# Performance work log

Measured on AMD Instinct MI355X. Metric: run time of the kernel, lower is better.

## Reference

```python
import jax, jax.numpy as jnp
import numpy as np

B, S, H, D = 2, 2048, 32, 128
DM = H * D  # 4096
SCALE = D ** -0.5


def setup_inputs() -> dict:
    key = jax.random.key(0)
    ks = jax.random.split(key, 7)
    std = DM ** -0.5
    return {
        "q": jax.random.normal(ks[0], (B, S, DM), dtype=jnp.float32),
        "k": jax.random.normal(ks[1], (B, S, DM), dtype=jnp.float32),
        "v": jax.random.normal(ks[2], (B, S, DM), dtype=jnp.float32),
        # torch nn.Linear weights are [out_features, in_features]
        "Wq": jax.random.normal(ks[3], (DM, DM), dtype=jnp.float32) * std,
        "Wk": jax.random.normal(ks[4], (DM, DM), dtype=jnp.float32) * std,
        "Wv": jax.random.normal(ks[5], (DM, DM), dtype=jnp.float32) * std,
        "Wo": jax.random.normal(ks[6], (DM, DM), dtype=jnp.float32) * std,
    }


def reference(q, k, v, Wq, Wk, Wv, Wo):
    # Linear: y = x @ W^T (no bias, qkv_bias=False)
    qp = q @ Wq.T  # [B,S,DM]
    kp = k @ Wk.T
    vp = v @ Wv.T
    # [B,S,DM] -> [B,H,S,D]
    qh = qp.reshape(B, S, H, D).transpose(0, 2, 1, 3)
    kh = kp.reshape(B, S, H, D).transpose(0, 2, 1, 3)
    vh = vp.reshape(B, S, H, D).transpose(0, 2, 1, 3)
    # scaled dot-product attention (no mask; attn_mask default None)
    scores = jnp.einsum("bhqd,bhkd->bhqk", qh, kh) * SCALE  # [B,H,S,S]
    probs = jax.nn.softmax(scores, axis=-1)
    ctx = jnp.einsum("bhqk,bhkd->bhqd", probs, vh)  # [B,H,S,D]
    ctx = ctx.transpose(0, 2, 1, 3).reshape(B, S, DM)
    return ctx @ Wo.T  # [B,S,DM]
```

## Files before the change

### kernel.cpp

```cpp
#include <hip/hip_runtime.h>
#include <hip/hip_bf16.h>
#include <stdint.h>


using u16 = unsigned short;
using u32 = unsigned int;

typedef __attribute__((ext_vector_type(8))) short bf16x8;
typedef __attribute__((ext_vector_type(8))) u16 u16x8;
typedef __attribute__((ext_vector_type(4))) float f32x4;

#define MFMA_BF16(A, B, C) __builtin_amdgcn_mfma_f32_16x16x32_bf16((A), (B), (C), 0, 0, 0)

static constexpr int kS = 2048, kDM = 4096, kD = 128;
static constexpr size_t kMat = (size_t)4096 * 4096;
static constexpr float kScaleLog2e = 0.08838834764831845f * 1.44269504088896340736f;

static __device__ __forceinline__ void gload_lds16(const u16* g, u16* l) {
  __builtin_amdgcn_global_load_lds((const __attribute__((address_space(1))) void*)g,
                                   (__attribute__((address_space(3))) void*)l, 16, 0, 0);
}

static __device__ __forceinline__ u16 f2bf(float f) {
  u32 u = __float_as_uint(f);
  u32 r = u + 0x7FFFu + ((u >> 16) & 1u);
  return (u16)(r >> 16);
}

static __device__ __forceinline__ float bf2f(u16 x) {
  return __uint_as_float((u32)x << 16);
}

static __device__ __forceinline__ u16 nbf(float f) {
  union { __hip_bfloat16 h; u16 u; } cv;
  cv.h = __float2bfloat16(f);
  return cv.u;
}

static __device__ __forceinline__ u16x8 cvt8(float4 a, float4 b) {
  u16x8 r;
  r[0] = f2bf(a.x); r[1] = f2bf(a.y); r[2] = f2bf(a.z); r[3] = f2bf(a.w);
  r[4] = f2bf(b.x); r[5] = f2bf(b.y); r[6] = f2bf(b.z); r[7] = f2bf(b.w);
  return r;
}

__global__ __launch_bounds__(256) void cvt_kernel(
    const float* __restrict__ s0, const float* __restrict__ s1,
    const float* __restrict__ s2, const float* __restrict__ s3,
    const float* __restrict__ s4, const float* __restrict__ s5,
    const float* __restrict__ s6, u16* __restrict__ dst) {
  const int y = blockIdx.y;
  const float* s = (y == 0) ? s0 : (y == 1) ? s1 : (y == 2) ? s2 : (y == 3) ? s3
                  : (y == 4) ? s4 : (y == 5) ? s5 : s6;
  u16* d = dst + (size_t)y * kMat;
  const size_t nchunk = kMat / 8;
  const size_t step = (size_t)gridDim.x * 256;
  for (size_t c = (size_t)blockIdx.x * 256 + threadIdx.x; c < nchunk; c += step) {
    const float* p = s + c * 8;
    float4 a = *(const float4*)p;
    float4 b = *(const float4*)(p + 4);
    *(u16x8*)(d + c * 8) = cvt8(a, b);
  }
}

template <bool TRANS, bool OUT_F32>
static __device__ __forceinline__ void gemm256(const u16* __restrict__ X,
                                               const u16* __restrict__ W,
                                               void* __restrict__ Yv,
                                               u16* __restrict__ lds) {
  constexpr int NT = kDM / 64;
  const int tid = threadIdx.x;
  const int lane = tid & 63;
  const int w = tid >> 6;
  const int fr = lane & 15;
  const int fq = lane >> 4;
  const int wr = w >> 2;
  const int wc = w & 3;
  const int m0 = blockIdx.y * 256;
  const int n0 = blockIdx.x * 256;

  const int srow = tid >> 3;
  const int scol = ((tid & 7) ^ (srow & 7)) * 8;
  const u16* Xrow = X + (size_t)(m0 + srow) * kDM + scol;
  const u16* Wrow = W + (size_t)(n0 + srow) * kDM + scol;
  const int w512 = w * 512;

  const int rBb = wc * 64 + fr;
  const int rAb = wr * 128 + fr;
  const int swz = fr & 7;

  f32x4 acc[8][4] = {};

#define STAGE2(ROWP, qrow, k0, ldq)                                       \
  do {                                                                    \
    gload_lds16((ROWP) + (size_t)(qrow) * kDM + (k0), &lds[(ldq) + w512]); \
    gload_lds16((ROWP) + (size_t)((qrow) + 64) * kDM + (k0),              \
                &lds[(ldq) + 4096 + w512]);                               \
  } while (0)

  STAGE2(Wrow, 0, 0, 0);
  STAGE2(Wrow, 128, 0, 8192);
  STAGE2(Xrow, 0, 0, 16384);
  STAGE2(Xrow, 128, 0, 24576);
  STAGE2(Wrow, 0, 64, 32768);
  STAGE2(Wrow, 128, 64, 32768 + 8192);
  STAGE2(Xrow, 0, 64, 32768 + 16384);
  asm volatile("s_waitcnt vmcnt(6)" ::: "memory");
  __builtin_amdgcn_s_barrier();

  for (int t = 0; t < NT; ++t) {
    const int d = t & 1;
    const int Boff = d * 32768;
    const int Aoff = Boff + 16384;
    bf16x8 bfr[4][2], af[8][2];

#pragma unroll
    for (int nf = 0; nf < 4; ++nf)
#pragma unroll
      for (int ks = 0; ks < 2; ++ks)
        bfr[nf][ks] = *(const bf16x8*)&lds[Boff + (rBb + nf * 16) * 64 +
                                           (((ks * 4 + fq) ^ swz) * 8)];
#pragma unroll
    for (int mi = 0; mi < 4; ++mi)
#pragma unroll
      for (int ks = 0; ks < 2; ++ks)
        af[mi][ks] = *(const bf16x8*)&lds[Aoff + (rAb + mi * 16) * 64 +
                                          (((ks * 4 + fq) ^ swz) * 8)];
    if (t + 1 < NT) STAGE2(Xrow, 128, (t + 1) * 64, ((t + 1) & 1) * 32768 + 24576);
    __builtin_amdgcn_s_barrier();
    __builtin_amdgcn_s_setprio(1);
#pragma unroll
    for (int mi = 0; mi < 2; ++mi)
#pragma unroll
      for (int nf = 0; nf < 4; ++nf)
#pragma unroll
        for (int ks = 0; ks < 2; ++ks)
          acc[mi][nf] = TRANS ? MFMA_BF16(bfr[nf][ks], af[mi][ks], acc[mi][nf])
                              : MFMA_BF16(af[mi][ks], bfr[nf][ks], acc[mi][nf]);
    __builtin_amdgcn_s_setprio(0);
    __builtin_amdgcn_s_barrier();

#pragma unroll
    for (int mi = 4; mi < 6; ++mi)
#pragma unroll
      for (int ks = 0; ks < 2; ++ks)
        af[mi][ks] = *(const bf16x8*)&lds[Aoff + (rAb + mi * 16) * 64 +
                                          (((ks * 4 + fq) ^ swz) * 8)];
    if (t + 2 < NT) STAGE2(Wrow, 0, (t + 2) * 64, d * 32768 + 0);
    __builtin_amdgcn_s_barrier();
    __builtin_amdgcn_s_setprio(1);
#pragma unroll
    for (int mi = 2; mi < 4; ++mi)
#pragma unroll
      for (int nf = 0; nf < 4; ++nf)
#pragma unroll
        for (int ks = 0; ks < 2; ++ks)
          acc[mi][nf] = TRANS ? MFMA_BF16(bfr[nf][ks], af[mi][ks], acc[mi][nf])
                              : MFMA_BF16(af[mi][ks], bfr[nf][ks], acc[mi][nf]);
    __builtin_amdgcn_s_setprio(0);
    __builtin_amdgcn_s_barrier();

#pragma unroll
    for (int mi = 6; mi < 8; ++mi)
#pragma unroll
      for (int ks = 0; ks < 2; ++ks)
        af[mi][ks] = *(const bf16x8*)&lds[Aoff + (rAb + mi * 16) * 64 +
                                          (((ks * 4 + fq) ^ swz) * 8)];
    if (t + 2 < NT) STAGE2(Wrow, 128, (t + 2) * 64, d * 32768 + 8192);
    __builtin_amdgcn_s_barrier();
    __builtin_amdgcn_s_setprio(1);
#pragma unroll
    for (int mi = 4; mi < 6; ++mi)
#pragma unroll
      for (int nf = 0; nf < 4; ++nf)
#pragma unroll
        for (int ks = 0; ks < 2; ++ks)
          acc[mi][nf] = TRANS ? MFMA_BF16(bfr[nf][ks], af[mi][ks], acc[mi][nf])
                              : MFMA_BF16(af[mi][ks], bfr[nf][ks], acc[mi][nf]);
    __builtin_amdgcn_s_setprio(0);
    asm volatile("s_waitcnt lgkmcnt(0)" ::: "memory");
    __builtin_amdgcn_s_barrier();

    if (t + 2 < NT) STAGE2(Xrow, 0, (t + 2) * 64, d * 32768 + 16384);
    __builtin_amdgcn_s_barrier();
    __builtin_amdgcn_s_setprio(1);
#pragma unroll
    for (int mi = 6; mi < 8; ++mi)
#pragma unroll
      for (int nf = 0; nf < 4; ++nf)
#pragma unroll
        for (int ks = 0; ks < 2; ++ks)
          acc[mi][nf] = TRANS ? MFMA_BF16(bfr[nf][ks], af[mi][ks], acc[mi][nf])
                              : MFMA_BF16(af[mi][ks], bfr[nf][ks], acc[mi][nf]);
    __builtin_amdgcn_s_setprio(0);
    if (t + 2 < NT)
      asm volatile("s_waitcnt vmcnt(6)" ::: "memory");
    else
      asm volatile("s_waitcnt vmcnt(0)" ::: "memory");
    __builtin_amdgcn_s_barrier();
  }
#undef STAGE2

#pragma unroll
  for (int mi = 0; mi < 8; ++mi)
#pragma unroll
    for (int nf = 0; nf < 4; ++nf) {
      int row, col;
      if constexpr (TRANS) {
        row = n0 + wc * 64 + nf * 16 + fq * 4;
        col = m0 + wr * 128 + mi * 16 + fr;
      } else {
        row = m0 + wr * 128 + mi * 16 + fq * 4;
        col = n0 + wc * 64 + nf * 16 + fr;
      }
      if constexpr (OUT_F32) {
        float* yp = (float*)Yv + (size_t)row * kDM + col;
#pragma unroll
        for (int i = 0; i < 4; ++i) yp[(size_t)i * kDM] = acc[mi][nf][i];
      } else {
        u16* yp = (u16*)Yv + (size_t)row * kDM + col;
#pragma unroll
        for (int i = 0; i < 4; ++i) yp[(size_t)i * kDM] = f2bf(acc[mi][nf][i]);
      }
    }
}

__global__ __launch_bounds__(512, 2) void proj_qk256_kernel(const u16* __restrict__ wsb,
                                                            u16* __restrict__ qp,
                                                            u16* __restrict__ kp) {
  __shared__ u16 lds[65536];
  const int z = blockIdx.z;
  gemm256<false, false>(wsb + (size_t)z * kMat, wsb + (size_t)(3 + z) * kMat,
                        z ? kp : qp, lds);
}

__global__ __launch_bounds__(512, 2) void proj_vT256_kernel(const u16* __restrict__ wsb,
                                                            u16* __restrict__ vpT) {
  __shared__ u16 lds[65536];
  gemm256<true, false>(wsb + 2 * kMat, wsb + 5 * kMat, vpT, lds);
}

__global__ __launch_bounds__(512, 2) void out_proj256_kernel(const u16* __restrict__ ctx,
                                                             const u16* __restrict__ Wob,
                                                             float* __restrict__ out) {
  __shared__ u16 lds[65536];
  gemm256<false, true>(ctx, Wob, out, lds);
}

template <bool A_BF16, bool TRANS, bool OUT_F32>
static __device__ __forceinline__ void gemm_conv(const void* Xv, const float* Wf,
                                                 void* Yv, u16* __restrict__ Als,
                                                 u16* __restrict__ Bls) {
  constexpr int KD = 4096;
  const int tid = threadIdx.x;
  const int lane = tid & 63;
  const int w = tid >> 6;
  const int fr = lane & 15;
  const int fq = lane >> 4;
  const int m0 = blockIdx.y * 128;
  const int n0 = blockIdx.x * 128;

  const int r0 = tid >> 2, cc0 = (tid & 3) * 8;
  const int r1 = r0 + 64;
  const int sr = lane >> 2, sc = (lane & 3) * 8;
  const int u0 = w * 2, u1 = w * 2 + 1;

  const u16* Xb = (const u16*)Xv;
  const float* Xf = (const float*)Xv;

  const int wm = (w >> 1) * 64;
  const int wn = (w & 1) * 64;

  f32x4 acc[4][4] = {};

  for (int kt = 0; kt < KD / 32; ++kt) {
    const int ko = kt * 32;
    if constexpr (A_BF16) {
      gload_lds16(Xb + (size_t)(m0 + u0 * 16 + sr) * KD + ko + sc, &Als[u0 * 512]);
      gload_lds16(Xb + (size_t)(m0 + u1 * 16 + sr) * KD + ko + sc, &Als[u1 * 512]);
    } else {
      const float* p0 = Xf + (size_t)(m0 + r0) * KD + ko + cc0;
      const float* p1 = Xf + (size_t)(m0 + r1) * KD + ko + cc0;
      float4 a0 = *(const float4*)(p0);
      float4 a1 = *(const float4*)(p0 + 4);
      float4 a2 = *(const float4*)(p1);
      float4 a3 = *(const float4*)(p1 + 4);
      *(u16x8*)&Als[r0 * 32 + cc0] = cvt8(a0, a1);
      *(u16x8*)&Als[r1 * 32 + cc0] = cvt8(a2, a3);
    }
    {
      const float* p0 = Wf + (size_t)(n0 + r0) * KD + ko + cc0;
      const float* p1 = Wf + (size_t)(n0 + r1) * KD + ko + cc0;
      float4 b0 = *(const float4*)(p0);
      float4 b1 = *(const float4*)(p0 + 4);
      float4 b2 = *(const float4*)(p1);
      float4 b3 = *(const float4*)(p1 + 4);
      *(u16x8*)&Bls[r0 * 32 + cc0] = cvt8(b0, b1);
      *(u16x8*)&Bls[r1 * 32 + cc0] = cvt8(b2, b3);
    }
    __syncthreads();

    bf16x8 af[4], bfv[4];
#pragma unroll
    for (int i = 0; i < 4; ++i)
      af[i] = *(const bf16x8*)&Als[(wm + i * 16 + fr) * 32 + fq * 8];
#pragma unroll
    for (int i = 0; i < 4; ++i)
      bfv[i] = *(const bf16x8*)&Bls[(wn + i * 16 + fr) * 32 + fq * 8];
#pragma unroll
    for (int a = 0; a < 4; ++a)
#pragma unroll
      for (int bb = 0; bb < 4; ++bb) {
        if constexpr (TRANS)
          acc[a][bb] = MFMA_BF16(bfv[a], af[bb], acc[a][bb]);
        else
          acc[a][bb] = MFMA_BF16(af[a], bfv[bb], acc[a][bb]);
      }
    __syncthreads();
  }

#pragma unroll
  for (int a = 0; a < 4; ++a)
#pragma unroll
    for (int bb = 0; bb < 4; ++bb) {
      const int row = TRANS ? (n0 + wn + a * 16 + fq * 4) : (m0 + wm + a * 16 + fq * 4);
      const int col = TRANS ? (m0 + wm + bb * 16 + fr) : (n0 + wn + bb * 16 + fr);
      if constexpr (OUT_F32) {
        float* yp = (float*)Yv + (size_t)row * kDM + col;
#pragma unroll
        for (int i = 0; i < 4; ++i) yp[(size_t)i * kDM] = acc[a][bb][i];
      } else {
        u16* yp = (u16*)Yv + (size_t)row * kDM + col;
#pragma unroll
        for (int i = 0; i < 4; ++i) yp[(size_t)i * kDM] = f2bf(acc[a][bb][i]);
      }
    }
}

__global__ __launch_bounds__(256) void proj_qk_conv_kernel(
    const float* __restrict__ q, const float* __restrict__ k,
    const float* __restrict__ Wq, const float* __restrict__ Wk,
    u16* __restrict__ qp, u16* __restrict__ kp) {
  __shared__ u16 Als[128 * 32];
  __shared__ u16 Bls[128 * 32];
  const int z = blockIdx.z;
  gemm_conv<false, false, false>(z ? k : q, z ? Wk : Wq, z ? kp : qp, Als, Bls);
}

__global__ __launch_bounds__(256) void proj_vT_conv_kernel(
    const float* __restrict__ v, const float* __restrict__ Wv, u16* __restrict__ vpT) {
  __shared__ u16 Als[128 * 32];
  __shared__ u16 Bls[128 * 32];
  gemm_conv<false, true, false>(v, Wv, vpT, Als, Bls);
}

__global__ __launch_bounds__(256) void out_proj_conv_kernel(const u16* __restrict__ ctx,
                                                            const float* __restrict__ Wo,
                                                            float* __restrict__ out) {
  __shared__ u16 Als[128 * 32];
  __shared__ u16 Bls[128 * 32];
  gemm_conv<true, false, true>(ctx, Wo, out, Als, Bls);
}

__global__ __launch_bounds__(512) void attn_kernel(const u16* __restrict__ qp,
                                                   const u16* __restrict__ kp,
                                                   const u16* __restrict__ vpT,
                                                   u16* __restrict__ ctx) {
  constexpr int KB = 64;
  constexpr int PST = 72;
  constexpr float THR = 11.5f;

  __shared__ u16 Kls[KB * 128];
  __shared__ u16 Vt[kD * KB];
  __shared__ u16 Pls[8][2 * 16 * PST];

  const int tid = threadIdx.x, lane = tid & 63, w = tid >> 6;
  const int fr = lane & 15, fq = lane >> 4;
  const int bh = blockIdx.y;
  const int b = bh >> 5, h = bh & 31;
  const int q0 = blockIdx.x * 256;

  const u16* qbase = qp + ((size_t)b * kS) * kDM + h * kD;
  const u16* kbase = kp + ((size_t)b * kS) * kDM + h * kD;
  const u16* vtbase = vpT + (size_t)(h * kD) * kDM + b * kS;

  bf16x8 qf[2][4];
#pragma unroll
  for (int rb = 0; rb < 2; ++rb)
#pragma unroll
    for (int kc = 0; kc < 4; ++kc) {
      const u16x8 raw = *(const u16x8*)(qbase +
          (size_t)(q0 + w * 32 + rb * 16 + fr) * kDM + kc * 32 + fq * 8);
      bf16x8 s;
#pragma unroll
      for (int j = 0; j < 8; ++j) s[j] = (short)f2bf(bf2f(raw[j]) * kScaleLog2e);
      qf[rb][kc] = s;
    }

  f32x4 oacc[2][8] = {};
  float mrun[2][4], lrun[2][4];
#pragma unroll
  for (int rb = 0; rb < 2; ++rb)
#pragma unroll
    for (int i = 0; i < 4; ++i) {
      mrun[rb][i] = -1e30f;
      lrun[rb][i] = 0.f;
    }

  const int krl = lane >> 4;
  const int kdp = lane & 15;
  const int vdl = lane >> 3;
  const int vc = lane & 7;

  for (int kt = 0; kt < kS / KB; ++kt) {
    const int kr0 = kt * KB;
#pragma unroll
    for (int t = 0; t < 2; ++t) {
      const int u = w * 2 + t;
      const int r = u * 4 + krl;
      const int dps = kdp ^ (r & 7);
      gload_lds16(kbase + (size_t)(kr0 + r) * kDM + dps * 8, &Kls[u * 512]);
    }
#pragma unroll
    for (int t = 0; t < 2; ++t) {
      const int u = w * 2 + t;
      const int d = u * 8 + vdl;
      gload_lds16(vtbase + (size_t)d * kDM + kr0 + ((vc ^ (d & 7)) * 8), &Vt[u * 512]);
    }
    __syncthreads();

    f32x4 sacc[2][4] = {};
#pragma unroll
    for (int cb = 0; cb < 4; ++cb) {
      const int n = cb * 16 + fr;
      bf16x8 kf[4];
#pragma unroll
      for (int kc = 0; kc < 4; ++kc) {
        const int d0 = kc * 4 + fq;
        kf[kc] = *(const bf16x8*)&Kls[n * 128 + (d0 ^ (n & 7)) * 8];
      }
      __builtin_amdgcn_s_setprio(1);
#pragma unroll
      for (int rb = 0; rb < 2; ++rb)
#pragma unroll
        for (int kc = 0; kc < 4; ++kc)
          sacc[rb][cb] = MFMA_BF16(qf[rb][kc], kf[kc], sacc[rb][cb]);
      __builtin_amdgcn_s_setprio(0);
    }

#pragma unroll
    for (int rb = 0; rb < 2; ++rb) {
      float mt[4];
#pragma unroll
      for (int i = 0; i < 4; ++i)
        mt[i] = fmaxf(fmaxf(sacc[rb][0][i], sacc[rb][1][i]),
                      fmaxf(sacc[rb][2][i], sacc[rb][3][i]));
#pragma unroll
      for (int off = 1; off < 16; off <<= 1)
#pragma unroll
        for (int i = 0; i < 4; ++i) mt[i] = fmaxf(mt[i], __shfl_xor(mt[i], off));

      const float grow = fmaxf(fmaxf(mt[0] - mrun[rb][0], mt[1] - mrun[rb][1]),
                               fmaxf(mt[2] - mrun[rb][2], mt[3] - mrun[rb][3]));
      if (__any(grow > THR)) {
        float scl[4];
#pragma unroll
        for (int i = 0; i < 4; ++i) {
          const float mnew = fmaxf(mrun[rb][i], mt[i]);
          scl[i] = exp2f(mrun[rb][i] - mnew);
          mrun[rb][i] = mnew;
          lrun[rb][i] *= scl[i];
        }
#pragma unroll
        for (int db = 0; db < 8; ++db)
#pragma unroll
          for (int i = 0; i < 4; ++i) oacc[rb][db][i] *= scl[i];
      }

      float rsum[4] = {0.f, 0.f, 0.f, 0.f};
#pragma unroll
      for (int cb = 0; cb < 4; ++cb)
#pragma unroll
        for (int i = 0; i < 4; ++i) {
          const float p = exp2f(sacc[rb][cb][i] - mrun[rb][i]);
          rsum[i] += p;
          Pls[w][rb * (16 * PST) + (fq * 4 + i) * PST + cb * 16 + fr] = nbf(p);
        }
#pragma unroll
      for (int off = 1; off < 16; off <<= 1)
#pragma unroll
        for (int i = 0; i < 4; ++i) rsum[i] += __shfl_xor(rsum[i], off);
#pragma unroll
      for (int i = 0; i < 4; ++i) lrun[rb][i] += rsum[i];
    }

    asm volatile("s_waitcnt lgkmcnt(0)" ::: "memory");

    bf16x8 pf[2][2];
#pragma unroll
    for (int rb = 0; rb < 2; ++rb)
#pragma unroll
      for (int kb = 0; kb < 2; ++kb)
        pf[rb][kb] = *(const bf16x8*)&Pls[w][rb * (16 * PST) + fr * PST + kb * 32 + fq * 8];
#pragma unroll
    for (int db = 0; db < 8; ++db) {
      const int d = db * 16 + fr;
      bf16x8 vf0 = *(const bf16x8*)&Vt[d * KB + ((fq ^ (d & 7)) << 3)];
      bf16x8 vf1 = *(const bf16x8*)&Vt[d * KB + (((4 + fq) ^ (d & 7)) << 3)];
      __builtin_amdgcn_s_setprio(1);
#pragma unroll
      for (int rb = 0; rb < 2; ++rb) {
        oacc[rb][db] = MFMA_BF16(pf[rb][0], vf0, oacc[rb][db]);
        oacc[rb][db] = MFMA_BF16(pf[rb][1], vf1, oacc[rb][db]);
      }
      __builtin_amdgcn_s_setprio(0);
    }
    __syncthreads();
  }

  u16* cbase = ctx + ((size_t)b * kS) * kDM + h * kD;
#pragma unroll
  for (int rb = 0; rb < 2; ++rb) {
    float inv[4];
#pragma unroll
    for (int i = 0; i < 4; ++i) inv[i] = 1.0f / lrun[rb][i];
#pragma unroll
    for (int db = 0; db < 8; ++db)
#pragma unroll
      for (int i = 0; i < 4; ++i) {
        const int row = q0 + w * 32 + rb * 16 + fq * 4 + i;
        const int col = db * 16 + fr;
        cbase[(size_t)row * kDM + col] = nbf(oacc[rb][db][i] * inv[i]);
      }
  }
}

extern "C" void kernel_launch(void* const* d_in, const int* in_sizes, int n_in,
                              void* d_out, int out_size, void* d_ws, size_t ws_size,
                              hipStream_t stream) {
  const float* q = (const float*)d_in[0];
  const float* k = (const float*)d_in[1];
  const float* v = (const float*)d_in[2];
  const float* Wq = (const float*)d_in[3];
  const float* Wk = (const float*)d_in[4];
  const float* Wv = (const float*)d_in[5];
  const float* Wo = (const float*)d_in[6];
  float* out = (float*)d_out;

  const size_t needFast = 11 * kMat * sizeof(u16);

  if (ws_size >= needFast) {
    u16* wsb = (u16*)d_ws;
    u16* qp = wsb + 7 * kMat;
    u16* kp = wsb + 8 * kMat;
    u16* vpT = wsb + 9 * kMat;
    u16* ctx = wsb + 10 * kMat;

    cvt_kernel<<<dim3(1024, 7), 256, 0, stream>>>(q, k, v, Wq, Wk, Wv, Wo, wsb);
    proj_qk256_kernel<<<dim3(16, 16, 2), 512, 0, stream>>>(wsb, qp, kp);
    proj_vT256_kernel<<<dim3(16, 16), 512, 0, stream>>>(wsb, vpT);
    attn_kernel<<<dim3(8, 64), 512, 0, stream>>>(qp, kp, vpT, ctx);
    out_proj256_kernel<<<dim3(16, 16), 512, 0, stream>>>(ctx, wsb + 6 * kMat, out);
  } else {
    u16* qp = (u16*)d_ws;
    u16* kp = qp + kMat;
    u16* vpT = kp + kMat;
    u16* ctx = vpT + kMat;

    proj_qk_conv_kernel<<<dim3(32, 32, 2), 256, 0, stream>>>(q, k, Wq, Wk, qp, kp);
    proj_vT_conv_kernel<<<dim3(32, 32), 256, 0, stream>>>(v, Wv, vpT);
    attn_kernel<<<dim3(8, 64), 512, 0, stream>>>(qp, kp, vpT, ctx);
    out_proj_conv_kernel<<<dim3(32, 32, 1), 256, 0, stream>>>(ctx, Wo, out);
  }
}
```

Measured before the change: 830.4 us.

## Prefetch K/V tiles through registers, compute row sums via MFMA, remap blocks

The attention kernel now loads the next K/V tile into registers while the current tile is being computed, then writes it to LDS after a barrier. This replaces the direct global-to-LDS loads that were followed by a sync. The softmax row-sum reduction, which used shuffles, is replaced by an extra MFMA of P against a ones vector, accumulated in a ninth oacc slot. Blocks are also remapped so that consecutive workgroups spread across heads, which may change L2 locality. The cost is more registers and an additional barrier per iteration.

```diff
diff --git a/kernel.cpp b/kernel.cpp
--- a/kernel.cpp
+++ b/kernel.cpp
@@ -367,6 +367,7 @@
                                                    const u16* __restrict__ vpT,
                                                    u16* __restrict__ ctx) {
   constexpr int KB = 64;
+  constexpr int NT = kS / KB;
   constexpr int PST = 72;
   constexpr float THR = 11.5f;
 
@@ -376,9 +377,12 @@
 
   const int tid = threadIdx.x, lane = tid & 63, w = tid >> 6;
   const int fr = lane & 15, fq = lane >> 4;
-  const int bh = blockIdx.y;
+
+  const int wg = blockIdx.y * 8 + blockIdx.x;
+  const int o = (wg & 7) * 64 + (wg >> 3);
+  const int bh = o >> 3;
   const int b = bh >> 5, h = bh & 31;
-  const int q0 = blockIdx.x * 256;
+  const int q0 = (o & 7) * 256;
 
   const u16* qbase = qp + ((size_t)b * kS) * kDM + h * kD;
   const u16* kbase = kp + ((size_t)b * kS) * kDM + h * kD;
@@ -397,37 +401,49 @@
       qf[rb][kc] = s;
     }
 
-  f32x4 oacc[2][8] = {};
-  float mrun[2][4], lrun[2][4];
+  f32x4 oacc[2][9] = {};
+  float mrun[2][4];
 #pragma unroll
   for (int rb = 0; rb < 2; ++rb)
 #pragma unroll
-    for (int i = 0; i < 4; ++i) {
-      mrun[rb][i] = -1e30f;
-      lrun[rb][i] = 0.f;
-    }
-
-  const int krl = lane >> 4;
-  const int kdp = lane & 15;
-  const int vdl = lane >> 3;
-  const int vc = lane & 7;
-
-  for (int kt = 0; kt < kS / KB; ++kt) {
-    const int kr0 = kt * KB;
-#pragma unroll
-    for (int t = 0; t < 2; ++t) {
-      const int u = w * 2 + t;
-      const int r = u * 4 + krl;
-      const int dps = kdp ^ (r & 7);
-      gload_lds16(kbase + (size_t)(kr0 + r) * kDM + dps * 8, &Kls[u * 512]);
-    }
-#pragma unroll
-    for (int t = 0; t < 2; ++t) {
-      const int u = w * 2 + t;
-      const int d = u * 8 + vdl;
-      gload_lds16(vtbase + (size_t)d * kDM + kr0 + ((vc ^ (d & 7)) * 8), &Vt[u * 512]);
-    }
-    __syncthreads();
+    for (int i = 0; i < 4; ++i) mrun[rb][i] = -1e30f;
+
+  bf16x8 ones;
+#pragma unroll
+  for (int j = 0; j < 8; ++j) ones[j] = (short)0x3F80;
+
+  const int krl = lane >> 4, kdp = lane & 15;
+  const int vdl = lane >> 3, vc = lane & 7;
+  const int rk0 = (w * 2 + 0) * 4 + krl;
+  const int rk1 = (w * 2 + 1) * 4 + krl;
+  const int dv0 = (w * 2 + 0) * 8 + vdl;
+  const int dv1 = (w * 2 + 1) * 8 + vdl;
+  const u16* kg0 = kbase + (size_t)rk0 * kDM + kdp * 8;
+  const u16* kg1 = kbase + (size_t)rk1 * kDM + kdp * 8;
+  const u16* vg0 = vtbase + (size_t)dv0 * kDM + vc * 8;
+  const u16* vg1 = vtbase + (size_t)dv1 * kDM + vc * 8;
+  u16* kl0 = &Kls[rk0 * 128 + ((kdp ^ (rk0 & 7)) * 8)];
+  u16* kl1 = &Kls[rk1 * 128 + ((kdp ^ (rk1 & 7)) * 8)];
+  u16* vl0 = &Vt[dv0 * KB + ((vc ^ (dv0 & 7)) * 8)];
+  u16* vl1 = &Vt[dv1 * KB + ((vc ^ (dv1 & 7)) * 8)];
+
+  u16x8 kr0v, kr1v, vr0v, vr1v;
+  kr0v = *(const u16x8*)kg0;
+  kr1v = *(const u16x8*)kg1;
+  vr0v = *(const u16x8*)vg0;
+  vr1v = *(const u16x8*)vg1;
+  *(u16x8*)kl0 = kr0v; *(u16x8*)kl1 = kr1v;
+  *(u16x8*)vl0 = vr0v; *(u16x8*)vl1 = vr1v;
+  __syncthreads();
+
+  for (int kt = 0; kt < NT; ++kt) {
+    if (kt + 1 < NT) {
+      const size_t ko = (size_t)(kt + 1) * KB;
+      kr0v = *(const u16x8*)(kg0 + ko * kDM);
+      kr1v = *(const u16x8*)(kg1 + ko * kDM);
+      vr0v = *(const u16x8*)(vg0 + ko);
+      vr1v = *(const u16x8*)(vg1 + ko);
+    }
 
     f32x4 sacc[2][4] = {};
 #pragma unroll
@@ -469,29 +485,20 @@
           const float mnew = fmaxf(mrun[rb][i], mt[i]);
           scl[i] = exp2f(mrun[rb][i] - mnew);
           mrun[rb][i] = mnew;
-          lrun[rb][i] *= scl[i];
         }
 #pragma unroll
-        for (int db = 0; db < 8; ++db)
+        for (int db = 0; db < 9; ++db)
 #pragma unroll
           for (int i = 0; i < 4; ++i) oacc[rb][db][i] *= scl[i];
       }
 
-      float rsum[4] = {0.f, 0.f, 0.f, 0.f};
 #pragma unroll
       for (int cb = 0; cb < 4; ++cb)
 #pragma unroll
         for (int i = 0; i < 4; ++i) {
           const float p = exp2f(sacc[rb][cb][i] - mrun[rb][i]);
-          rsum[i] += p;
           Pls[w][rb * (16 * PST) + (fq * 4 + i) * PST + cb * 16 + fr] = nbf(p);
         }
-#pragma unroll
-      for (int off = 1; off < 16; off <<= 1)
-#pragma unroll
-        for (int i = 0; i < 4; ++i) rsum[i] += __shfl_xor(rsum[i], off);
-#pragma unroll
-      for (int i = 0; i < 4; ++i) lrun[rb][i] += rsum[i];
     }
 
     asm volatile("s_waitcnt lgkmcnt(0)" ::: "memory");
@@ -515,6 +522,19 @@
       }
       __builtin_amdgcn_s_setprio(0);
     }
+    __builtin_amdgcn_s_setprio(1);
+#pragma unroll
+    for (int rb = 0; rb < 2; ++rb) {
+      oacc[rb][8] = MFMA_BF16(pf[rb][0], ones, oacc[rb][8]);
+      oacc[rb][8] = MFMA_BF16(pf[rb][1], ones, oacc[rb][8]);
+    }
+    __builtin_amdgcn_s_setprio(0);
+
+    __syncthreads();
+    if (kt + 1 < NT) {
+      *(u16x8*)kl0 = kr0v; *(u16x8*)kl1 = kr1v;
+      *(u16x8*)vl0 = vr0v; *(u16x8*)vl1 = vr1v;
+    }
     __syncthreads();
   }
 
@@ -523,7 +543,7 @@
   for (int rb = 0; rb < 2; ++rb) {
     float inv[4];
 #pragma unroll
-    for (int i = 0; i < 4; ++i) inv[i] = 1.0f / lrun[rb][i];
+    for (int i = 0; i < 4; ++i) inv[i] = 1.0f / oacc[rb][8][i];
 #pragma unroll
     for (int db = 0; db < 8; ++db)
 #pragma unroll
```

Measured after the change: 775.4 us. 1.07x faster.
